# Performance work log

Hardware: AMD Instinct MI355X
Metric: run time of the kernel (lower is better)

The kernel has to match this reference:

```python
import jax, jax.numpy as jnp
import numpy as np


def setup_inputs() -> dict:
    key = jax.random.key(0)
    k1, k2 = jax.random.split(key)
    B, N, M = 8, 4096, 4096
    points1 = jax.random.normal(k1, (B, N, 3), dtype=jnp.float32)
    points2 = jax.random.normal(k2, (B, M, 3), dtype=jnp.float32)
    return {"points1": points1, "points2": points2}


def reference(points1, points2):
    x2 = jnp.sum(points1 * points1, axis=-1)            # [B, N]
    y2 = jnp.sum(points2 * points2, axis=-1)            # [B, M]
    xy = jnp.einsum('bnd,bmd->bnm', points1, points2)   # [B, N, M]
    d = x2[:, :, None] + y2[:, None, :] - 2.0 * xy      # [B, N, M]
    dist1 = jnp.min(d, axis=2)                          # [B, N] NN dist p1->p2
    dist2 = jnp.min(d, axis=1)                          # [B, M] NN dist p2->p1
    # Symmetric Hausdorff: max over each direction, then max of the two, sum over batch
    m = jnp.maximum(jnp.max(dist1, axis=-1), jnp.max(dist2, axis=-1))  # [B]
    return jnp.sum(m)
```

## Files before the change

### kernel.cpp

```cpp
#include <hip/hip_runtime.h>
#include <float.h>

#define B_CONST 8
#define GROUPS 4
#define FLT_MAX_BITS 0x7F7FFFFFu

typedef float v2f __attribute__((ext_vector_type(2)));

__global__ void hd_pack(const float* __restrict__ p1, const float* __restrict__ p2,
                        float4* __restrict__ o1, float4* __restrict__ o2,
                        unsigned int* __restrict__ qmin, unsigned int* __restrict__ bmax,
                        int n1, int n2) {
    int i = blockIdx.x * blockDim.x + threadIdx.x;
    if (i < n1 + n2) qmin[i] = FLT_MAX_BITS;
    if (blockIdx.x == 0 && threadIdx.x < B_CONST + 1)
        bmax[threadIdx.x] = 0u;
    const float* src; float4* dst; int idx;
    if (i < n1)           { src = p1; dst = o1; idx = i; }
    else if (i < n1 + n2) { src = p2; dst = o2; idx = i - n1; }
    else return;
    size_t s = 3 * (size_t)idx;
    float x = src[s], y = src[s + 1], z = src[s + 2];
    dst[idx] = make_float4(x, y, z, fmaf(x, x, fmaf(y, y, z * z)));
}

__global__ __launch_bounds__(512) void hd_nnmax(
    const float4* __restrict__ qpt1, const float4* __restrict__ qpt2,
    unsigned int* __restrict__ qmin, int N, int M, int blocksDir0) {
    int blk = blockIdx.x;
    const float4* q; const float4* r; int QN, RM; unsigned int* qm;
    if (blk < blocksDir0) { q = qpt1; r = qpt2; QN = N; RM = M; qm = qmin; }
    else { blk -= blocksDir0; q = qpt2; r = qpt1; QN = M; RM = N; qm = qmin + B_CONST * N; }

    int qblocks = QN >> 9;
    int perB = qblocks * GROUPS;
    int b    = blk / perB;
    int rem  = blk - b * perB;
    int qblk = rem / GROUPS;
    int g    = rem - qblk * GROUPS;

    int l = threadIdx.x & 63;
    int w = __builtin_amdgcn_readfirstlane((int)(threadIdx.x >> 6));

    const float4* qb = q + (size_t)b * QN + ((size_t)qblk << 9);
    float4 qv[8];
    #pragma unroll
    for (int s = 0; s < 8; ++s) qv[s] = qb[s * 64 + l];
    v2f NX[4], NY[4], NZ[4], MN[4];
    #pragma unroll
    for (int p = 0; p < 4; ++p) {
        NX[p] = (v2f){ -2.0f * qv[2*p].x, -2.0f * qv[2*p+1].x };
        NY[p] = (v2f){ -2.0f * qv[2*p].y, -2.0f * qv[2*p+1].y };
        NZ[p] = (v2f){ -2.0f * qv[2*p].z, -2.0f * qv[2*p+1].z };
        MN[p] = (v2f){ FLT_MAX, FLT_MAX };
    }

    int cnt = RM >> 5;
    const float4* rb = r + (size_t)b * RM + (size_t)g * (RM >> 2) + (size_t)w * cnt;

    #pragma unroll 8
    for (int j = 0; j < cnt; ++j) {
        float4 rf = rb[j];
        v2f rx = (v2f){ rf.x, rf.x };
        v2f ry = (v2f){ rf.y, rf.y };
        v2f rz = (v2f){ rf.z, rf.z };
        v2f rw = (v2f){ rf.w, rf.w };
        #pragma unroll
        for (int p = 0; p < 4; ++p) {
            v2f a = __builtin_elementwise_fma(NX[p], rx, rw);
            a = __builtin_elementwise_fma(NY[p], ry, a);
            a = __builtin_elementwise_fma(NZ[p], rz, a);
            MN[p] = __builtin_elementwise_min(MN[p], a);
        }
    }

    __shared__ float red[4096];
    #pragma unroll
    for (int p = 0; p < 4; ++p) {
        red[(w << 9) + (2*p)     * 64 + l] = MN[p].x;
        red[(w << 9) + (2*p + 1) * 64 + l] = MN[p].y;
    }
    __syncthreads();
    int t = threadIdx.x;
    float m = red[t];
    #pragma unroll
    for (int ww = 1; ww < 8; ++ww) m = fminf(m, red[(ww << 9) + t]);
    float4 qq = qb[t];
    float dist = fmaxf(qq.w + m, 0.0f);
    atomicMin(qm + (size_t)b * QN + ((size_t)qblk << 9) + t, __float_as_uint(dist));
}

__global__ __launch_bounds__(256) void hd_final(
    const unsigned int* __restrict__ qmin, unsigned int* __restrict__ bmax,
    float* __restrict__ out, int N, int M) {
    int dir = blockIdx.x >> 3;
    int b   = blockIdx.x & 7;
    int cnt = dir ? M : N;
    const unsigned int* src = qmin + (dir ? (size_t)B_CONST * N + (size_t)b * M
                                          : (size_t)b * N);
    unsigned int mx = 0u;
    for (int i = threadIdx.x; i < cnt; i += 256) mx = max(mx, src[i]);
    #pragma unroll
    for (int off = 32; off > 0; off >>= 1)
        mx = max(mx, (unsigned int)__shfl_down((int)mx, off, 64));
    __shared__ unsigned int wmax[4];
    if ((threadIdx.x & 63) == 0) wmax[threadIdx.x >> 6] = mx;
    __syncthreads();
    if (threadIdx.x == 0) {
        mx = max(max(wmax[0], wmax[1]), max(wmax[2], wmax[3]));
        atomicMax(&bmax[b], mx);
        __threadfence();
        unsigned int ticket = atomicAdd(&bmax[B_CONST], 1u);
        if (ticket == 15u) {
            float s = 0.0f;
            for (int bb = 0; bb < B_CONST; ++bb)
                s += __uint_as_float(atomicMax(&bmax[bb], 0u));
            out[0] = s;
        }
    }
}

extern "C" void kernel_launch(void* const* d_in, const int* in_sizes, int n_in,
                              void* d_out, int out_size, void* d_ws, size_t ws_size,
                              hipStream_t stream) {
    const float* p1 = (const float*)d_in[0];
    const float* p2 = (const float*)d_in[1];
    const int B = B_CONST;
    int N = in_sizes[0] / (3 * B);
    int M = in_sizes[1] / (3 * B);
    int n1 = B * N, n2 = B * M;

    char* ws = (char*)d_ws;
    float4* qpt1 = (float4*)ws;
    float4* qpt2 = (float4*)(ws + (size_t)n1 * sizeof(float4));
    unsigned int* qmin = (unsigned int*)(ws + (size_t)(n1 + n2) * sizeof(float4));
    unsigned int* bmax = qmin + (n1 + n2);

    int packBlocks = (n1 + n2 + 255) / 256;
    hd_pack<<<packBlocks, 256, 0, stream>>>(p1, p2, qpt1, qpt2, qmin, bmax, n1, n2);

    int blocksDir0 = B * (N >> 9) * GROUPS;
    int blocksDir1 = B * (M >> 9) * GROUPS;
    hd_nnmax<<<blocksDir0 + blocksDir1, 512, 0, stream>>>(qpt1, qpt2, qmin, N, M, blocksDir0);

    hd_final<<<16, 256, 0, stream>>>(qmin, bmax, (float*)d_out, N, M);
}
```

Before: 83.68 us.

## Fuse final reduction into NN kernel via last-block ticket and per-group partials

Per-query atomicMin into a shared qmin array is replaced by plain stores of per-group partial minima into a separate buffer. A per-(direction,batch) ticket counter then picks the last finishing block, which reduces the group minima and the max, and does the batch sum. This removes the third kernel launch, the qmin initialisation writes and the global atomics. In exchange it adds a fence, a ticket atomic per block and a serial tail reduction of 4096x4 values in one block per batch.

```diff
diff --git a/kernel.cpp b/kernel.cpp
--- a/kernel.cpp
+++ b/kernel.cpp
@@ -3,18 +3,18 @@
 
 #define B_CONST 8
 #define GROUPS 4
-#define FLT_MAX_BITS 0x7F7FFFFFu
 
 typedef float v2f __attribute__((ext_vector_type(2)));
 
+__device__ __forceinline__ float coh_load(const float* p) {
+    return __hip_atomic_load(p, __ATOMIC_RELAXED, __HIP_MEMORY_SCOPE_AGENT);
+}
+
 __global__ void hd_pack(const float* __restrict__ p1, const float* __restrict__ p2,
                         float4* __restrict__ o1, float4* __restrict__ o2,
-                        unsigned int* __restrict__ qmin, unsigned int* __restrict__ bmax,
-                        int n1, int n2) {
+                        unsigned int* __restrict__ comm, int n1, int n2) {
     int i = blockIdx.x * blockDim.x + threadIdx.x;
-    if (i < n1 + n2) qmin[i] = FLT_MAX_BITS;
-    if (blockIdx.x == 0 && threadIdx.x < B_CONST + 1)
-        bmax[threadIdx.x] = 0u;
+    if (blockIdx.x == 0 && threadIdx.x < 25) comm[threadIdx.x] = 0u;
     const float* src; float4* dst; int idx;
     if (i < n1)           { src = p1; dst = o1; idx = i; }
     else if (i < n1 + n2) { src = p2; dst = o2; idx = i - n1; }
@@ -26,11 +26,12 @@
 
 __global__ __launch_bounds__(512) void hd_nnmax(
     const float4* __restrict__ qpt1, const float4* __restrict__ qpt2,
-    unsigned int* __restrict__ qmin, int N, int M, int blocksDir0) {
+    float* __restrict__ part, unsigned int* __restrict__ comm,
+    float* __restrict__ out, int N, int M, int blocksDir0) {
     int blk = blockIdx.x;
-    const float4* q; const float4* r; int QN, RM; unsigned int* qm;
-    if (blk < blocksDir0) { q = qpt1; r = qpt2; QN = N; RM = M; qm = qmin; }
-    else { blk -= blocksDir0; q = qpt2; r = qpt1; QN = M; RM = N; qm = qmin + B_CONST * N; }
+    const float4* q; const float4* r; int QN, RM, dir;
+    if (blk < blocksDir0) { q = qpt1; r = qpt2; QN = N; RM = M; dir = 0; }
+    else { blk -= blocksDir0; q = qpt2; r = qpt1; QN = M; RM = N; dir = 1; }
 
     int qblocks = QN >> 9;
     int perB = qblocks * GROUPS;
@@ -85,36 +86,46 @@
     float m = red[t];
     #pragma unroll
     for (int ww = 1; ww < 8; ++ww) m = fminf(m, red[(ww << 9) + t]);
-    float4 qq = qb[t];
-    float dist = fmaxf(qq.w + m, 0.0f);
-    atomicMin(qm + (size_t)b * QN + ((size_t)qblk << 9) + t, __float_as_uint(dist));
-}
+    float dist = fmaxf(qb[t].w + m, 0.0f);
 
-__global__ __launch_bounds__(256) void hd_final(
-    const unsigned int* __restrict__ qmin, unsigned int* __restrict__ bmax,
-    float* __restrict__ out, int N, int M) {
-    int dir = blockIdx.x >> 3;
-    int b   = blockIdx.x & 7;
-    int cnt = dir ? M : N;
-    const unsigned int* src = qmin + (dir ? (size_t)B_CONST * N + (size_t)b * M
-                                          : (size_t)b * N);
-    unsigned int mx = 0u;
-    for (int i = threadIdx.x; i < cnt; i += 256) mx = max(mx, src[i]);
+    size_t dirOff = dir ? (size_t)GROUPS * B_CONST * N : 0;
+    float* pb = part + dirOff + ((size_t)g * B_CONST + b) * QN;
+    pb[((size_t)qblk << 9) + t] = dist;
+
+    __threadfence();
+    __syncthreads();
+    __shared__ unsigned int sTicket;
+    int db = dir * B_CONST + b;
+    if (threadIdx.x == 0) sTicket = atomicAdd(&comm[9 + db], 1u);
+    __syncthreads();
+    if (sTicket + 1u != (unsigned int)perB) return;
+
+    const float* fb = part + dirOff + (size_t)b * QN;
+    size_t gs = (size_t)B_CONST * QN;
+    float mx = 0.0f;
+    for (int qq = threadIdx.x; qq < QN; qq += 512) {
+        float mm = coh_load(fb + qq);
+        #pragma unroll
+        for (int gg = 1; gg < GROUPS; ++gg)
+            mm = fminf(mm, coh_load(fb + gg * gs + qq));
+        mx = fmaxf(mx, mm);
+    }
     #pragma unroll
     for (int off = 32; off > 0; off >>= 1)
-        mx = max(mx, (unsigned int)__shfl_down((int)mx, off, 64));
-    __shared__ unsigned int wmax[4];
-    if ((threadIdx.x & 63) == 0) wmax[threadIdx.x >> 6] = mx;
+        mx = fmaxf(mx, __shfl_down(mx, off, 64));
+    __shared__ float wred[8];
+    if (l == 0) wred[w] = mx;
     __syncthreads();
     if (threadIdx.x == 0) {
-        mx = max(max(wmax[0], wmax[1]), max(wmax[2], wmax[3]));
-        atomicMax(&bmax[b], mx);
+        #pragma unroll
+        for (int ww = 1; ww < 8; ++ww) mx = fmaxf(mx, wred[ww]);
+        atomicMax(&comm[b], __float_as_uint(mx));
         __threadfence();
-        unsigned int ticket = atomicAdd(&bmax[B_CONST], 1u);
-        if (ticket == 15u) {
+        unsigned int t2 = atomicAdd(&comm[8], 1u);
+        if (t2 == 15u) {
             float s = 0.0f;
             for (int bb = 0; bb < B_CONST; ++bb)
-                s += __uint_as_float(atomicMax(&bmax[bb], 0u));
+                s += __uint_as_float(atomicMax(&comm[bb], 0u));
             out[0] = s;
         }
     }
@@ -133,15 +144,14 @@
     char* ws = (char*)d_ws;
     float4* qpt1 = (float4*)ws;
     float4* qpt2 = (float4*)(ws + (size_t)n1 * sizeof(float4));
-    unsigned int* qmin = (unsigned int*)(ws + (size_t)(n1 + n2) * sizeof(float4));
-    unsigned int* bmax = qmin + (n1 + n2);
+    float* part  = (float*)(ws + (size_t)(n1 + n2) * sizeof(float4));
+    unsigned int* comm = (unsigned int*)(part + (size_t)GROUPS * (n1 + n2));
 
     int packBlocks = (n1 + n2 + 255) / 256;
-    hd_pack<<<packBlocks, 256, 0, stream>>>(p1, p2, qpt1, qpt2, qmin, bmax, n1, n2);
+    hd_pack<<<packBlocks, 256, 0, stream>>>(p1, p2, qpt1, qpt2, comm, n1, n2);
 
     int blocksDir0 = B * (N >> 9) * GROUPS;
     int blocksDir1 = B * (M >> 9) * GROUPS;
-    hd_nnmax<<<blocksDir0 + blocksDir1, 512, 0, stream>>>(qpt1, qpt2, qmin, N, M, blocksDir0);
-
-    hd_final<<<16, 256, 0, stream>>>(qmin, bmax, (float*)d_out, N, M);
+    hd_nnmax<<<blocksDir0 + blocksDir1, 512, 0, stream>>>(
+        qpt1, qpt2, part, comm, (float*)d_out, N, M, blocksDir0);
 }
```

New measurement: 148.8 us. 77.8% more time.
